# Performance work log

Hardware: AMD Instinct MI355X
Metric: run time of the kernel (lower is better)

## Reference

```python
import jax, jax.numpy as jnp
import numpy as np

N_NODES, N_EDGES, H = 25000, 400000, 64
EPS = 1e-15


def _norm(x):
    return jnp.sqrt(jnp.sum(x * x, axis=-1, keepdims=True))


def _projx(x, c):
    norm = _norm(x)
    max_norm = (1.0 - 1e-5) / jnp.sqrt(c)
    scale = jnp.minimum(max_norm / jnp.maximum(norm, EPS), 1.0)
    return x * scale


def _expmap0(x, c):
    norm = _norm(x)
    sc = jnp.sqrt(c)
    return jnp.tanh(sc * norm) * x / (norm * sc + EPS)


def _logmap0(x, c):
    norm = _norm(x)
    sc = jnp.sqrt(c)
    return (1.0 / sc) * jnp.arctanh(jnp.minimum(sc * norm, 1.0 - 1e-5)) * x / (norm + EPS)


def _mobius_add(x, y, c):
    x2 = jnp.sum(x * x, axis=-1, keepdims=True)
    y2 = jnp.sum(y * y, axis=-1, keepdims=True)
    xy = jnp.sum(x * y, axis=-1, keepdims=True)
    num = (1.0 + 2.0 * c * xy + c * y2) * x + (1.0 - c * x2) * y
    denom = 1.0 + 2.0 * c * xy + c * c * x2 * y2
    return num / (denom + EPS)


def _mobius_linear(x, W, b, c):
    t = _logmap0(x, c)
    out = t @ W.T + b
    return _expmap0(out, c)


def setup_inputs() -> dict:
    key = jax.random.key(0)
    ks = jax.random.split(key, 12)
    h_V = jax.random.normal(ks[0], (N_NODES, H), dtype=jnp.float32) * 0.3
    h_E = jax.random.normal(ks[1], (N_EDGES, 3 * H), dtype=jnp.float32) * 0.3
    src = jax.random.randint(ks[2], (N_EDGES,), 0, N_NODES, dtype=jnp.int32)
    dst = jax.random.randint(ks[3], (N_EDGES,), 0, N_NODES, dtype=jnp.int32)
    log_c = jnp.zeros((), dtype=jnp.float32)  # c = 1.0

    def lin(k, out_d, in_d):
        bound = 1.0 / np.sqrt(in_d)
        kw, kb = jax.random.split(k)
        W = jax.random.uniform(kw, (out_d, in_d), jnp.float32, -bound, bound)
        b = jax.random.uniform(kb, (out_d,), jnp.float32, -bound, bound)
        return W, b

    W1_w, W1_b = lin(ks[4], H, 5 * H)
    W2_w, W2_b = lin(ks[5], H, H)
    W3_w, W3_b = lin(ks[6], H, H)
    return {"h_V": h_V, "h_E": h_E, "src": src, "dst": dst, "log_c": log_c,
            "W1_w": W1_w, "W1_b": W1_b, "W2_w": W2_w, "W2_b": W2_b,
            "W3_w": W3_w, "W3_b": W3_b}


def reference(h_V, h_E, src, dst, log_c, W1_w, W1_b, W2_w, W2_b, W3_w, W3_b):
    c = jnp.exp(log_c)
    n_nodes = h_V.shape[0]
    h_E = _projx(h_E, c)
    h_V = _projx(h_V, c)
    # edge gather -> fused mobius-linear chain  [E, 5H] -> [E, H]
    h_EV = jnp.concatenate([h_E, h_V[src], h_V[dst]], axis=-1)
    h_EV = _mobius_linear(h_EV, W1_w, W1_b, c)
    h_EV = _mobius_linear(_projx(jax.nn.relu(h_EV), c), W2_w, W2_b, c)
    h_msg = _mobius_linear(_projx(jax.nn.relu(h_EV), c), W3_w, W3_b, c)
    # hyperbolic aggregate: logmap0 -> scatter-mean over src -> expmap0
    tangent = _logmap0(h_msg, c)
    sums = jax.ops.segment_sum(tangent, src, num_segments=n_nodes)
    counts = jax.ops.segment_sum(jnp.ones((tangent.shape[0],), tangent.dtype), src,
                                 num_segments=n_nodes)
    agg_t = sums / jnp.maximum(counts, 1.0)[:, None]
    agg = _expmap0(agg_t, c)
    h_V = _mobius_add(h_V, agg, c)  # dropout disabled (eval)
    return _projx(h_V, c)
```

## Files before the change

kernel.cpp:

```cpp
#include <hip/hip_runtime.h>
#include <hip/hip_bf16.h>
#include <math.h>

#define EPSF 1e-15f

typedef __attribute__((ext_vector_type(8))) short bf16x8;
typedef __attribute__((ext_vector_type(16))) float f32x16;

__device__ __forceinline__ unsigned short f2bf(float x) {
    unsigned u = __float_as_uint(x);
    u += 0x7fffu + ((u >> 16) & 1u);
    return (unsigned short)(u >> 16);
}
__device__ __forceinline__ float bf2f(unsigned short b) {
    return __uint_as_float(((unsigned)b) << 16);
}
__device__ __forceinline__ unsigned pkbf(float lo, float hi) {
    __hip_bfloat162 h = __float22bfloat162_rn(make_float2(lo, hi));
    return *reinterpret_cast<unsigned*>(&h);
}
__device__ __forceinline__ float fast_tanh_pos(float x) {
    if (x < 0.25f) { float x2 = x * x; return x * (1.0f - x2 * (0.33333334f - 0.13333334f * x2)); }
    float e = __expf(2.0f * x);
    return 1.0f - 2.0f / (e + 1.0f);
}
__device__ __forceinline__ float fast_atanh01(float y) {
    if (y < 0.125f) { float y2 = y * y; return y * (1.0f + y2 * (0.33333334f + 0.2f * y2)); }
    return 0.5f * __logf((1.0f + y) / (1.0f - y));
}

__device__ __forceinline__ float wred(float v) {
#pragma unroll
    for (int off = 32; off; off >>= 1) v += __shfl_xor(v, off);
    return v;
}

__global__ void prep_wfrag(const float* __restrict__ W1, const float* __restrict__ W2,
                           const float* __restrict__ W3, unsigned short* __restrict__ Wf) {
    int idx = blockIdx.x * blockDim.x + threadIdx.x;
    if (idx >= 56 * 64) return;
    int fid = idx >> 6, lane = idx & 63;
    int e31 = lane & 31, hi = lane >> 5;
    unsigned short* dstp = Wf + ((size_t)fid * 64 + lane) * 8;
    if (fid < 40) {
        int ks = fid >> 1, t = fid & 1;
        int n = 32 * t + e31;
        int k0 = 16 * ks + 8 * hi;
#pragma unroll
        for (int i = 0; i < 8; ++i) dstp[i] = f2bf(W1[n * 320 + k0 + i]);
    } else {
        const float* srcW = (fid < 48) ? W2 : W3;
        int b = (fid < 48) ? fid - 40 : fid - 48;
        int ks = b >> 1, t2 = b & 1;
        int n = 32 * t2 + e31;
        int cb = 32 * (ks >> 1) + 16 * (ks & 1) + 4 * hi;
#pragma unroll
        for (int i = 0; i < 8; ++i) dstp[i] = f2bf(srcW[n * 64 + cb + 8 * (i >> 2) + (i & 3)]);
    }
}

__global__ void __launch_bounds__(256)
node_prep(const float* __restrict__ hV, const float* __restrict__ logc,
          unsigned short* __restrict__ hVp, float* __restrict__ pj, int n_nodes) {
    int wid  = (blockIdx.x * blockDim.x + threadIdx.x) >> 6;
    int lane = threadIdx.x & 63;
    if (wid >= n_nodes) return;
    float c    = __expf(logc[0]);
    float scq  = sqrtf(c);
    float maxn = (1.0f - 1e-5f) / scq;
    float x = hV[(size_t)wid * 64 + lane];
    float p = wred(x * x);
    float sS = fminf(maxn / fmaxf(sqrtf(p), EPSF), 1.0f);
    hVp[(size_t)wid * 64 + lane] = f2bf(x * sS);
    if (lane == 0) pj[wid] = sS * sS * p;
}

__global__ void hist_kernel(const int* __restrict__ src, int* __restrict__ cnt,
                            int* __restrict__ slot, int n_edges) {
    int e = blockIdx.x * blockDim.x + threadIdx.x;
    if (e < n_edges) slot[e] = atomicAdd(&cnt[src[e]], 1);
}

__global__ void __launch_bounds__(1024)
scan_rowptr(const int* __restrict__ cnt, int* __restrict__ rowptr, int n) {
    __shared__ int wpart[16];
    int C   = (n + 1023) >> 10;
    int tid = threadIdx.x;
    int beg = tid * C;
    int end = beg + C; if (end > n) end = n;
    int s = 0;
    if (beg < n) for (int k = beg; k < end; ++k) s += cnt[k];
    int lane = tid & 63, wv = tid >> 6;
    int v = s;
#pragma unroll
    for (int off = 1; off < 64; off <<= 1) {
        int t = __shfl_up(v, off);
        if (lane >= off) v += t;
    }
    if (lane == 63) wpart[wv] = v;
    __syncthreads();
    if (tid < 64) {
        int t = (tid < 16) ? wpart[tid] : 0;
#pragma unroll
        for (int off = 1; off < 16; off <<= 1) {
            int u = __shfl_up(t, off);
            if (lane >= off) t += u;
        }
        if (tid < 16) wpart[tid] = t;
    }
    __syncthreads();
    int base = (wv ? wpart[wv - 1] : 0) + (v - s);
    if (beg < n) {
        int run = base;
        for (int k = beg; k < end; ++k) { rowptr[k] = run; run += cnt[k]; }
    }
    if (tid == 1023) rowptr[n] = wpart[15];
}

__global__ void __launch_bounds__(256, 4)
gemm1e(const float* __restrict__ hE, const unsigned short* __restrict__ Wf,
       unsigned short* __restrict__ yEb, float* __restrict__ pEarr,
       int n_edges, int n_tiles) {
    int lane = threadIdx.x & 63;
    int w    = threadIdx.x >> 6;
    int tile = blockIdx.x * 4 + w;
    if (tile >= n_tiles) return;
    int e31 = lane & 31, hi = lane >> 5;
    int ev = tile * 32 + e31; if (ev >= n_edges) ev = n_edges - 1;

    const bf16x8* Wfrag = reinterpret_cast<const bf16x8*>(Wf);
    const float* eb = hE + (size_t)ev * 192 + 8 * hi;

    f32x16 acc[2] = {};
    float pE = 0.f;
#pragma unroll 1
    for (int ks = 0; ks < 12; ++ks) {
        const float4* p4 = reinterpret_cast<const float4*>(eb + 16 * ks);
        float4 a0 = p4[0], a1 = p4[1];
        pE += a0.x*a0.x + a0.y*a0.y + a0.z*a0.z + a0.w*a0.w
            + a1.x*a1.x + a1.y*a1.y + a1.z*a1.z + a1.w*a1.w;
        union { bf16x8 b; unsigned u[4]; } cv;
        cv.u[0] = pkbf(a0.x, a0.y);
        cv.u[1] = pkbf(a0.z, a0.w);
        cv.u[2] = pkbf(a1.x, a1.y);
        cv.u[3] = pkbf(a1.z, a1.w);
        acc[0] = __builtin_amdgcn_mfma_f32_32x32x16_bf16(
            Wfrag[(size_t)(ks * 2 + 0) * 64 + lane], cv.b, acc[0], 0, 0, 0);
        acc[1] = __builtin_amdgcn_mfma_f32_32x32x16_bf16(
            Wfrag[(size_t)(ks * 2 + 1) * 64 + lane], cv.b, acc[1], 0, 0, 0);
    }
    pE += __shfl_xor(pE, 32);

    unsigned pk[16];
#pragma unroll
    for (int t = 0; t < 2; ++t)
#pragma unroll
        for (int wd = 0; wd < 8; ++wd)
            pk[t * 8 + wd] = pkbf(acc[t][2 * wd], acc[t][2 * wd + 1]);
    uint4* op = reinterpret_cast<uint4*>(yEb + ((size_t)tile * 64 + lane) * 32);
    op[0] = make_uint4(pk[0],  pk[1],  pk[2],  pk[3]);
    op[1] = make_uint4(pk[4],  pk[5],  pk[6],  pk[7]);
    op[2] = make_uint4(pk[8],  pk[9],  pk[10], pk[11]);
    op[3] = make_uint4(pk[12], pk[13], pk[14], pk[15]);
    if (hi == 0 && tile * 32 + e31 < n_edges) pEarr[tile * 32 + e31] = pE;
}

__device__ __forceinline__ void stage_mlp32(float (&v)[2][16],
                                            const unsigned short* WfL, int fbase,
                                            const float* __restrict__ bvec,
                                            float scq, float maxn, int lane, int hi) {
    float n2 = 0.f, rn2 = 0.f;
    float u[2][16];
#pragma unroll
    for (int t = 0; t < 2; ++t)
#pragma unroll
        for (int j = 0; j < 16; ++j) {
            float x = v[t][j];
            n2 = fmaf(x, x, n2);
            float y = fmaxf(x, 0.f);
            u[t][j] = y;
            rn2 = fmaf(y, y, rn2);
        }
    n2  += __shfl_xor(n2, 32);
    rn2 += __shfl_xor(rn2, 32);
    float n  = sqrtf(n2);
    float h  = fast_tanh_pos(scq * n) / (n * scq + EPSF);
    float rn = h * sqrtf(rn2);
    float ps = fminf(maxn / fmaxf(rn, EPSF), 1.0f);
    float pn = rn * ps;
    float gg = fast_atanh01(fminf(scq * pn, 1.0f - 1e-5f)) / (scq * (pn + EPSF));
    float f2 = h * ps * gg;

    f32x16 acc[2] = {};
#pragma unroll
    for (int ks = 0; ks < 4; ++ks) {
        int t = ks >> 1, jb = 8 * (ks & 1);
        union { bf16x8 b; unsigned w[4]; } B;
        B.w[0] = pkbf(u[t][jb + 0], u[t][jb + 1]);
        B.w[1] = pkbf(u[t][jb + 2], u[t][jb + 3]);
        B.w[2] = pkbf(u[t][jb + 4], u[t][jb + 5]);
        B.w[3] = pkbf(u[t][jb + 6], u[t][jb + 7]);
#pragma unroll
        for (int t2 = 0; t2 < 2; ++t2) {
            bf16x8 wf = *reinterpret_cast<const bf16x8*>(
                &WfL[((fbase + ks * 2 + t2) * 64 + lane) * 8]);
            acc[t2] = __builtin_amdgcn_mfma_f32_32x32x16_bf16(wf, B.b, acc[t2], 0, 0, 0);
        }
    }
#pragma unroll
    for (int t2 = 0; t2 < 2; ++t2)
#pragma unroll
        for (int q = 0; q < 4; ++q) {
            const float4 bv = *reinterpret_cast<const float4*>(&bvec[32 * t2 + 8 * q + 4 * hi]);
            v[t2][4 * q + 0] = fmaf(f2, acc[t2][4 * q + 0], bv.x);
            v[t2][4 * q + 1] = fmaf(f2, acc[t2][4 * q + 1], bv.y);
            v[t2][4 * q + 2] = fmaf(f2, acc[t2][4 * q + 2], bv.z);
            v[t2][4 * q + 3] = fmaf(f2, acc[t2][4 * q + 3], bv.w);
        }
}

__global__ void __launch_bounds__(256, 4)
edge_mfma(const unsigned short* __restrict__ yEb, const float* __restrict__ pEarr,
          const int* __restrict__ src, const int* __restrict__ dst,
          const float* __restrict__ logc,
          const unsigned short* __restrict__ Wf, const unsigned short* __restrict__ hVp,
          const float* __restrict__ pj,
          const float* __restrict__ b1, const float* __restrict__ b2,
          const float* __restrict__ b3, const int* __restrict__ slot_,
          const int* __restrict__ rowptr,
          unsigned short* __restrict__ tg, int n_edges, int n_tiles) {
    __shared__ __align__(16) unsigned short WfL[16384];
    {
        const uint4* wsrc = reinterpret_cast<const uint4*>(Wf) + 1536;
        uint4* wdst = reinterpret_cast<uint4*>(WfL);
#pragma unroll
        for (int i = 0; i < 8; ++i)
            wdst[i * 256 + threadIdx.x] = wsrc[i * 256 + threadIdx.x];
    }
    __syncthreads();

    int lane = threadIdx.x & 63;
    int w    = threadIdx.x >> 6;
    int tile = blockIdx.x * 4 + w;
    if (tile >= n_tiles) return;

    float c    = __expf(logc[0]);
    float scq  = sqrtf(c);
    float maxn = (1.0f - 1e-5f) / scq;

    int e31 = lane & 31, hi = lane >> 5;
    int ev = tile * 32 + e31; if (ev >= n_edges) ev = n_edges - 1;
    int s16 = src[ev], d16 = dst[ev];
    int sl = slot_[ev] + rowptr[s16];
    float pjS = pj[s16], pjD = pj[d16];
    float pE  = pEarr[ev];

    const uint4* yp = reinterpret_cast<const uint4*>(yEb + ((size_t)tile * 64 + lane) * 32);
    uint4 y0 = yp[0], y1 = yp[1], y2 = yp[2], y3 = yp[3];
    unsigned yw[16] = { y0.x, y0.y, y0.z, y0.w, y1.x, y1.y, y1.z, y1.w,
                        y2.x, y2.y, y2.z, y2.w, y3.x, y3.y, y3.z, y3.w };

    const bf16x8* vsp = reinterpret_cast<const bf16x8*>(hVp + (size_t)s16 * 64);
    const bf16x8* vdp = reinterpret_cast<const bf16x8*>(hVp + (size_t)d16 * 64);
    bf16x8 aS[4], aD[4];
#pragma unroll
    for (int q = 0; q < 4; ++q) { aS[q] = vsp[2 * q + hi]; aD[q] = vdp[2 * q + hi]; }

    f32x16 accV[2] = {};
#pragma unroll
    for (int q = 0; q < 4; ++q) {
#pragma unroll
        for (int t = 0; t < 2; ++t) {
            bf16x8 wf = *reinterpret_cast<const bf16x8*>(&WfL[((q * 2 + t) * 64 + lane) * 8]);
            accV[t] = __builtin_amdgcn_mfma_f32_32x32x16_bf16(wf, aS[q], accV[t], 0, 0, 0);
        }
    }
#pragma unroll
    for (int q = 0; q < 4; ++q) {
#pragma unroll
        for (int t = 0; t < 2; ++t) {
            bf16x8 wf = *reinterpret_cast<const bf16x8*>(&WfL[((8 + q * 2 + t) * 64 + lane) * 8]);
            accV[t] = __builtin_amdgcn_mfma_f32_32x32x16_bf16(wf, aD[q], accV[t], 0, 0, 0);
        }
    }

    float sE = fminf(maxn / fmaxf(sqrtf(pE), EPSF), 1.0f);
    float nt = sqrtf(sE * sE * pE + pjS + pjD);
    float gq = fast_atanh01(fminf(scq * nt, 1.0f - 1e-5f)) / (scq * (nt + EPSF));

    float v[2][16];
#pragma unroll
    for (int t = 0; t < 2; ++t)
#pragma unroll
        for (int q = 0; q < 4; ++q) {
            const float4 bv = *reinterpret_cast<const float4*>(&b1[32 * t + 8 * q + 4 * hi]);
#pragma unroll
            for (int j = 0; j < 4; ++j) {
                int f = t * 16 + q * 4 + j;
                float ye = bf2f((unsigned short)(yw[f >> 1] >> (16 * (f & 1))));
                float bb = (j == 0) ? bv.x : (j == 1) ? bv.y : (j == 2) ? bv.z : bv.w;
                v[t][q * 4 + j] = fmaf(gq, fmaf(sE, ye, accV[t][q * 4 + j]), bb);
            }
        }

    stage_mlp32(v, WfL, 16, b2, scq, maxn, lane, hi);
    stage_mlp32(v, WfL, 24, b3, scq, maxn, lane, hi);

    float n2 = 0.f;
#pragma unroll
    for (int t = 0; t < 2; ++t)
#pragma unroll
        for (int j = 0; j < 16; ++j) n2 = fmaf(v[t][j], v[t][j], n2);
    n2 += __shfl_xor(n2, 32);
    float n  = sqrtf(n2);
    float h  = fast_tanh_pos(scq * n) / (n * scq + EPSF);
    float hn = h * n;
    float g4 = fast_atanh01(fminf(scq * hn, 1.0f - 1e-5f)) / (scq * (hn + EPSF));
    float fT = g4 * h;

    if (tile * 32 + e31 < n_edges) {
        unsigned short* orow = tg + (size_t)sl * 64;
#pragma unroll
        for (int t = 0; t < 2; ++t)
#pragma unroll
            for (int q = 0; q < 4; ++q) {
                uint2 o;
                o.x = pkbf(fT * v[t][4*q+0], fT * v[t][4*q+1]);
                o.y = pkbf(fT * v[t][4*q+2], fT * v[t][4*q+3]);
                *reinterpret_cast<uint2*>(&orow[32 * t + 8 * q + 4 * hi]) = o;
            }
    }
}

__global__ void __launch_bounds__(256)
node_gather(const float* __restrict__ hV, const float* __restrict__ logc,
            const unsigned short* __restrict__ tg, const int* __restrict__ rowptr,
            float* __restrict__ out, int n_nodes) {
    int wid  = (blockIdx.x * blockDim.x + threadIdx.x) >> 6;
    int lane = threadIdx.x & 63;
    if (wid >= n_nodes) return;

    float c    = __expf(logc[0]);
    float scq  = sqrtf(c);
    float maxn = (1.0f - 1e-5f) / scq;

    int beg = rowptr[wid], end = rowptr[wid + 1];
    int g = lane >> 4, i15 = lane & 15;
    float s0 = 0.f, s1 = 0.f, s2 = 0.f, s3 = 0.f;
    for (int i = beg + g; i < end; i += 4) {
        uint2 p = *reinterpret_cast<const uint2*>(&tg[(size_t)i * 64 + i15 * 4]);
        s0 += bf2f((unsigned short)(p.x & 0xffff));
        s1 += bf2f((unsigned short)(p.x >> 16));
        s2 += bf2f((unsigned short)(p.y & 0xffff));
        s3 += bf2f((unsigned short)(p.y >> 16));
    }
    s0 += __shfl_xor(s0, 16); s0 += __shfl_xor(s0, 32);
    s1 += __shfl_xor(s1, 16); s1 += __shfl_xor(s1, 32);
    s2 += __shfl_xor(s2, 16); s2 += __shfl_xor(s2, 32);
    s3 += __shfl_xor(s3, 16); s3 += __shfl_xor(s3, 32);
    int srcl = lane >> 2;
    float a0 = __shfl(s0, srcl), a1 = __shfl(s1, srcl);
    float a2 = __shfl(s2, srcl), a3 = __shfl(s3, srcl);
    float ssum = (lane & 2) ? ((lane & 1) ? a3 : a2) : ((lane & 1) ? a1 : a0);

    float inv = 1.f / fmaxf((float)(end - beg), 1.f);
    float at  = ssum * inv;

    float an2 = wred(at * at);
    float an  = sqrtf(an2);
    float ae  = fast_tanh_pos(scq * an) / (an * scq + EPSF);

    float xv  = hV[(size_t)wid * 64 + lane];
    float hs2 = wred(xv * xv);
    float sX  = fminf(maxn / fmaxf(sqrtf(hs2), EPSF), 1.0f);

    float x = sX * xv, y = ae * at;
    float x2 = wred(x * x);
    float y2 = wred(y * y);
    float xy = wred(x * y);

    float ca = 1.f + 2.f * c * xy + c * y2;
    float cb = 1.f - c * x2;
    float id = 1.f / (1.f + 2.f * c * xy + c * c * x2 * y2 + EPSF);

    float r   = (ca * x + cb * y) * id;
    float rn2 = wred(r * r);
    float rs  = fminf(maxn / fmaxf(sqrtf(rn2), EPSF), 1.0f);

    out[(size_t)wid * 64 + lane] = rs * r;
}

extern "C" void kernel_launch(void* const* d_in, const int* in_sizes, int n_in,
                              void* d_out, int out_size, void* d_ws, size_t ws_size,
                              hipStream_t stream) {
    const float* hV   = (const float*)d_in[0];
    const float* hE   = (const float*)d_in[1];
    const int*   src  = (const int*)d_in[2];
    const int*   dst  = (const int*)d_in[3];
    const float* logc = (const float*)d_in[4];
    const float* W1   = (const float*)d_in[5];
    const float* b1   = (const float*)d_in[6];
    const float* W2   = (const float*)d_in[7];
    const float* b2   = (const float*)d_in[8];
    const float* W3   = (const float*)d_in[9];
    const float* b3   = (const float*)d_in[10];

    int n_nodes = in_sizes[0] / 64;
    int n_edges = in_sizes[2];
    int n_tiles = (n_edges + 31) / 32;
    float* out = (float*)d_out;

    char* wsb = (char*)d_ws;
    unsigned short* Wf = (unsigned short*)wsb;
    size_t off = 56 * 512 * sizeof(unsigned short);
    int* cnt    = (int*)(wsb + off);   off += (size_t)n_nodes * 4;
    int* rowptr = (int*)(wsb + off);   off += (size_t)(n_nodes + 1) * 4;
    int* slot   = (int*)(wsb + off);   off += (size_t)n_edges * 4;
    float* pj   = (float*)(wsb + off); off += (size_t)n_nodes * 4;
    float* pEarr= (float*)(wsb + off); off += (size_t)n_edges * 4;
    off = (off + 15) & ~(size_t)15;
    unsigned short* hVp = (unsigned short*)(wsb + off);
    off += (size_t)n_nodes * 64 * 2;
    off = (off + 15) & ~(size_t)15;
    unsigned short* yEb = (unsigned short*)(wsb + off);
    off += (size_t)n_tiles * 64 * 32 * 2;
    off = (off + 15) & ~(size_t)15;
    unsigned short* tg = (unsigned short*)(wsb + off);

    hipMemsetAsync(cnt, 0, (size_t)n_nodes * sizeof(int), stream);

    prep_wfrag<<<(56 * 64 + 255) / 256, 256, 0, stream>>>(W1, W2, W3, Wf);
    node_prep<<<(n_nodes + 3) / 4, 256, 0, stream>>>(hV, logc, hVp, pj, n_nodes);
    hist_kernel<<<(n_edges + 255) / 256, 256, 0, stream>>>(src, cnt, slot, n_edges);
    scan_rowptr<<<1, 1024, 0, stream>>>(cnt, rowptr, n_nodes);

    gemm1e<<<(n_tiles + 3) / 4, 256, 0, stream>>>(hE, Wf, yEb, pEarr, n_edges, n_tiles);

    edge_mfma<<<(n_tiles + 3) / 4, 256, 0, stream>>>(
        yEb, pEarr, src, dst, logc, Wf, hVp, pj, b1, b2, b3, slot, rowptr,
        tg, n_edges, n_tiles);

    node_gather<<<(n_nodes + 3) / 4, 256, 0, stream>>>(
        hV, logc, tg, rowptr, out, n_nodes);
}
```

Baseline: 251.4 us.

## Fuse edge-feature GEMM into the edge MLP kernel, dropping intermediate buffers

Merges the separate h_E projection kernel into the main edge kernel, so the bf16 intermediate yE and the per-edge squared norm are kept in registers instead of being written to and reread from global memory. This removes one launch and a round trip of about 26MB of intermediate traffic. The fused kernel now carries both the E-part and V-part accumulators at once, which raises register pressure and may lower occupancy. The E-part accumulator is also no longer rounded to bf16 before use.

```diff
diff --git a/kernel.cpp b/kernel.cpp
--- a/kernel.cpp
+++ b/kernel.cpp
@@ -117,21 +117,119 @@
     if (tid == 1023) rowptr[n] = wpart[15];
 }
 
+__device__ __forceinline__ void stage_mlp32(float (&v)[2][16],
+                                            const unsigned short* WfL, int fbase,
+                                            const float* __restrict__ bvec,
+                                            float scq, float maxn, int lane, int hi) {
+    float n2 = 0.f, rn2 = 0.f;
+    float u[2][16];
+#pragma unroll
+    for (int t = 0; t < 2; ++t)
+#pragma unroll
+        for (int j = 0; j < 16; ++j) {
+            float x = v[t][j];
+            n2 = fmaf(x, x, n2);
+            float y = fmaxf(x, 0.f);
+            u[t][j] = y;
+            rn2 = fmaf(y, y, rn2);
+        }
+    n2  += __shfl_xor(n2, 32);
+    rn2 += __shfl_xor(rn2, 32);
+    float n  = sqrtf(n2);
+    float h  = fast_tanh_pos(scq * n) / (n * scq + EPSF);
+    float rn = h * sqrtf(rn2);
+    float ps = fminf(maxn / fmaxf(rn, EPSF), 1.0f);
+    float pn = rn * ps;
+    float gg = fast_atanh01(fminf(scq * pn, 1.0f - 1e-5f)) / (scq * (pn + EPSF));
+    float f2 = h * ps * gg;
+
+    f32x16 acc[2] = {};
+#pragma unroll
+    for (int ks = 0; ks < 4; ++ks) {
+        int t = ks >> 1, jb = 8 * (ks & 1);
+        union { bf16x8 b; unsigned w[4]; } B;
+        B.w[0] = pkbf(u[t][jb + 0], u[t][jb + 1]);
+        B.w[1] = pkbf(u[t][jb + 2], u[t][jb + 3]);
+        B.w[2] = pkbf(u[t][jb + 4], u[t][jb + 5]);
+        B.w[3] = pkbf(u[t][jb + 6], u[t][jb + 7]);
+#pragma unroll
+        for (int t2 = 0; t2 < 2; ++t2) {
+            bf16x8 wf = *reinterpret_cast<const bf16x8*>(
+                &WfL[((fbase + ks * 2 + t2) * 64 + lane) * 8]);
+            acc[t2] = __builtin_amdgcn_mfma_f32_32x32x16_bf16(wf, B.b, acc[t2], 0, 0, 0);
+        }
+    }
+#pragma unroll
+    for (int t2 = 0; t2 < 2; ++t2)
+#pragma unroll
+        for (int q = 0; q < 4; ++q) {
+            const float4 bv = *reinterpret_cast<const float4*>(&bvec[32 * t2 + 8 * q + 4 * hi]);
+            v[t2][4 * q + 0] = fmaf(f2, acc[t2][4 * q + 0], bv.x);
+            v[t2][4 * q + 1] = fmaf(f2, acc[t2][4 * q + 1], bv.y);
+            v[t2][4 * q + 2] = fmaf(f2, acc[t2][4 * q + 2], bv.z);
+            v[t2][4 * q + 3] = fmaf(f2, acc[t2][4 * q + 3], bv.w);
+        }
+}
+
 __global__ void __launch_bounds__(256, 4)
-gemm1e(const float* __restrict__ hE, const unsigned short* __restrict__ Wf,
-       unsigned short* __restrict__ yEb, float* __restrict__ pEarr,
-       int n_edges, int n_tiles) {
+edge_fused(const float* __restrict__ hE, const int* __restrict__ src,
+           const int* __restrict__ dst, const float* __restrict__ logc,
+           const unsigned short* __restrict__ Wf, const unsigned short* __restrict__ hVp,
+           const float* __restrict__ pj,
+           const float* __restrict__ b1, const float* __restrict__ b2,
+           const float* __restrict__ b3, const int* __restrict__ slot_,
+           const int* __restrict__ rowptr,
+           unsigned short* __restrict__ tg, int n_edges, int n_tiles) {
+    __shared__ __align__(16) unsigned short WfL[16384];
+    {
+        const uint4* wsrc = reinterpret_cast<const uint4*>(Wf) + 1536;
+        uint4* wdst = reinterpret_cast<uint4*>(WfL);
+#pragma unroll
+        for (int i = 0; i < 8; ++i)
+            wdst[i * 256 + threadIdx.x] = wsrc[i * 256 + threadIdx.x];
+    }
+    __syncthreads();
+
     int lane = threadIdx.x & 63;
     int w    = threadIdx.x >> 6;
     int tile = blockIdx.x * 4 + w;
     if (tile >= n_tiles) return;
+
+    float c    = __expf(logc[0]);
+    float scq  = sqrtf(c);
+    float maxn = (1.0f - 1e-5f) / scq;
+
     int e31 = lane & 31, hi = lane >> 5;
     int ev = tile * 32 + e31; if (ev >= n_edges) ev = n_edges - 1;
+    int s16 = src[ev], d16 = dst[ev];
+    int sl = slot_[ev] + rowptr[s16];
+    float pjS = pj[s16], pjD = pj[d16];
+
+    const bf16x8* vsp = reinterpret_cast<const bf16x8*>(hVp + (size_t)s16 * 64);
+    const bf16x8* vdp = reinterpret_cast<const bf16x8*>(hVp + (size_t)d16 * 64);
+    f32x16 accV[2] = {};
+#pragma unroll
+    for (int q = 0; q < 4; ++q) {
+        bf16x8 aS = vsp[2 * q + hi];
+#pragma unroll
+        for (int t = 0; t < 2; ++t) {
+            bf16x8 wf = *reinterpret_cast<const bf16x8*>(&WfL[((q * 2 + t) * 64 + lane) * 8]);
+            accV[t] = __builtin_amdgcn_mfma_f32_32x32x16_bf16(wf, aS, accV[t], 0, 0, 0);
+        }
+    }
+#pragma unroll
+    for (int q = 0; q < 4; ++q) {
+        bf16x8 aD = vdp[2 * q + hi];
+#pragma unroll
+        for (int t = 0; t < 2; ++t) {
+            bf16x8 wf = *reinterpret_cast<const bf16x8*>(&WfL[((8 + q * 2 + t) * 64 + lane) * 8]);
+            accV[t] = __builtin_amdgcn_mfma_f32_32x32x16_bf16(wf, aD, accV[t], 0, 0, 0);
+        }
+    }
 
     const bf16x8* Wfrag = reinterpret_cast<const bf16x8*>(Wf);
     const float* eb = hE + (size_t)ev * 192 + 8 * hi;
-
-    f32x16 acc[2] = {};
+    f32x16 accE[2] = {};
     float pE = 0.f;
 #pragma unroll 1
     for (int ks = 0; ks < 12; ++ks) {
@@ -144,145 +242,12 @@
         cv.u[1] = pkbf(a0.z, a0.w);
         cv.u[2] = pkbf(a1.x, a1.y);
         cv.u[3] = pkbf(a1.z, a1.w);
-        acc[0] = __builtin_amdgcn_mfma_f32_32x32x16_bf16(
-            Wfrag[(size_t)(ks * 2 + 0) * 64 + lane], cv.b, acc[0], 0, 0, 0);
-        acc[1] = __builtin_amdgcn_mfma_f32_32x32x16_bf16(
-            Wfrag[(size_t)(ks * 2 + 1) * 64 + lane], cv.b, acc[1], 0, 0, 0);
+        accE[0] = __builtin_amdgcn_mfma_f32_32x32x16_bf16(
+            Wfrag[(size_t)(ks * 2 + 0) * 64 + lane], cv.b, accE[0], 0, 0, 0);
+        accE[1] = __builtin_amdgcn_mfma_f32_32x32x16_bf16(
+            Wfrag[(size_t)(ks * 2 + 1) * 64 + lane], cv.b, accE[1], 0, 0, 0);
     }
     pE += __shfl_xor(pE, 32);
-
-    unsigned pk[16];
-#pragma unroll
-    for (int t = 0; t < 2; ++t)
-#pragma unroll
-        for (int wd = 0; wd < 8; ++wd)
-            pk[t * 8 + wd] = pkbf(acc[t][2 * wd], acc[t][2 * wd + 1]);
-    uint4* op = reinterpret_cast<uint4*>(yEb + ((size_t)tile * 64 + lane) * 32);
-    op[0] = make_uint4(pk[0],  pk[1],  pk[2],  pk[3]);
-    op[1] = make_uint4(pk[4],  pk[5],  pk[6],  pk[7]);
-    op[2] = make_uint4(pk[8],  pk[9],  pk[10], pk[11]);
-    op[3] = make_uint4(pk[12], pk[13], pk[14], pk[15]);
-    if (hi == 0 && tile * 32 + e31 < n_edges) pEarr[tile * 32 + e31] = pE;
-}
-
-__device__ __forceinline__ void stage_mlp32(float (&v)[2][16],
-                                            const unsigned short* WfL, int fbase,
-                                            const float* __restrict__ bvec,
-                                            float scq, float maxn, int lane, int hi) {
-    float n2 = 0.f, rn2 = 0.f;
-    float u[2][16];
-#pragma unroll
-    for (int t = 0; t < 2; ++t)
-#pragma unroll
-        for (int j = 0; j < 16; ++j) {
-            float x = v[t][j];
-            n2 = fmaf(x, x, n2);
-            float y = fmaxf(x, 0.f);
-            u[t][j] = y;
-            rn2 = fmaf(y, y, rn2);
-        }
-    n2  += __shfl_xor(n2, 32);
-    rn2 += __shfl_xor(rn2, 32);
-    float n  = sqrtf(n2);
-    float h  = fast_tanh_pos(scq * n) / (n * scq + EPSF);
-    float rn = h * sqrtf(rn2);
-    float ps = fminf(maxn / fmaxf(rn, EPSF), 1.0f);
-    float pn = rn * ps;
-    float gg = fast_atanh01(fminf(scq * pn, 1.0f - 1e-5f)) / (scq * (pn + EPSF));
-    float f2 = h * ps * gg;
-
-    f32x16 acc[2] = {};
-#pragma unroll
-    for (int ks = 0; ks < 4; ++ks) {
-        int t = ks >> 1, jb = 8 * (ks & 1);
-        union { bf16x8 b; unsigned w[4]; } B;
-        B.w[0] = pkbf(u[t][jb + 0], u[t][jb + 1]);
-        B.w[1] = pkbf(u[t][jb + 2], u[t][jb + 3]);
-        B.w[2] = pkbf(u[t][jb + 4], u[t][jb + 5]);
-        B.w[3] = pkbf(u[t][jb + 6], u[t][jb + 7]);
-#pragma unroll
-        for (int t2 = 0; t2 < 2; ++t2) {
-            bf16x8 wf = *reinterpret_cast<const bf16x8*>(
-                &WfL[((fbase + ks * 2 + t2) * 64 + lane) * 8]);
-            acc[t2] = __builtin_amdgcn_mfma_f32_32x32x16_bf16(wf, B.b, acc[t2], 0, 0, 0);
-        }
-    }
-#pragma unroll
-    for (int t2 = 0; t2 < 2; ++t2)
-#pragma unroll
-        for (int q = 0; q < 4; ++q) {
-            const float4 bv = *reinterpret_cast<const float4*>(&bvec[32 * t2 + 8 * q + 4 * hi]);
-            v[t2][4 * q + 0] = fmaf(f2, acc[t2][4 * q + 0], bv.x);
-            v[t2][4 * q + 1] = fmaf(f2, acc[t2][4 * q + 1], bv.y);
-            v[t2][4 * q + 2] = fmaf(f2, acc[t2][4 * q + 2], bv.z);
-            v[t2][4 * q + 3] = fmaf(f2, acc[t2][4 * q + 3], bv.w);
-        }
-}
-
-__global__ void __launch_bounds__(256, 4)
-edge_mfma(const unsigned short* __restrict__ yEb, const float* __restrict__ pEarr,
-          const int* __restrict__ src, const int* __restrict__ dst,
-          const float* __restrict__ logc,
-          const unsigned short* __restrict__ Wf, const unsigned short* __restrict__ hVp,
-          const float* __restrict__ pj,
-          const float* __restrict__ b1, const float* __restrict__ b2,
-          const float* __restrict__ b3, const int* __restrict__ slot_,
-          const int* __restrict__ rowptr,
-          unsigned short* __restrict__ tg, int n_edges, int n_tiles) {
-    __shared__ __align__(16) unsigned short WfL[16384];
-    {
-        const uint4* wsrc = reinterpret_cast<const uint4*>(Wf) + 1536;
-        uint4* wdst = reinterpret_cast<uint4*>(WfL);
-#pragma unroll
-        for (int i = 0; i < 8; ++i)
-            wdst[i * 256 + threadIdx.x] = wsrc[i * 256 + threadIdx.x];
-    }
-    __syncthreads();
-
-    int lane = threadIdx.x & 63;
-    int w    = threadIdx.x >> 6;
-    int tile = blockIdx.x * 4 + w;
-    if (tile >= n_tiles) return;
-
-    float c    = __expf(logc[0]);
-    float scq  = sqrtf(c);
-    float maxn = (1.0f - 1e-5f) / scq;
-
-    int e31 = lane & 31, hi = lane >> 5;
-    int ev = tile * 32 + e31; if (ev >= n_edges) ev = n_edges - 1;
-    int s16 = src[ev], d16 = dst[ev];
-    int sl = slot_[ev] + rowptr[s16];
-    float pjS = pj[s16], pjD = pj[d16];
-    float pE  = pEarr[ev];
-
-    const uint4* yp = reinterpret_cast<const uint4*>(yEb + ((size_t)tile * 64 + lane) * 32);
-    uint4 y0 = yp[0], y1 = yp[1], y2 = yp[2], y3 = yp[3];
-    unsigned yw[16] = { y0.x, y0.y, y0.z, y0.w, y1.x, y1.y, y1.z, y1.w,
-                        y2.x, y2.y, y2.z, y2.w, y3.x, y3.y, y3.z, y3.w };
-
-    const bf16x8* vsp = reinterpret_cast<const bf16x8*>(hVp + (size_t)s16 * 64);
-    const bf16x8* vdp = reinterpret_cast<const bf16x8*>(hVp + (size_t)d16 * 64);
-    bf16x8 aS[4], aD[4];
-#pragma unroll
-    for (int q = 0; q < 4; ++q) { aS[q] = vsp[2 * q + hi]; aD[q] = vdp[2 * q + hi]; }
-
-    f32x16 accV[2] = {};
-#pragma unroll
-    for (int q = 0; q < 4; ++q) {
-#pragma unroll
-        for (int t = 0; t < 2; ++t) {
-            bf16x8 wf = *reinterpret_cast<const bf16x8*>(&WfL[((q * 2 + t) * 64 + lane) * 8]);
-            accV[t] = __builtin_amdgcn_mfma_f32_32x32x16_bf16(wf, aS[q], accV[t], 0, 0, 0);
-        }
-    }
-#pragma unroll
-    for (int q = 0; q < 4; ++q) {
-#pragma unroll
-        for (int t = 0; t < 2; ++t) {
-            bf16x8 wf = *reinterpret_cast<const bf16x8*>(&WfL[((8 + q * 2 + t) * 64 + lane) * 8]);
-            accV[t] = __builtin_amdgcn_mfma_f32_32x32x16_bf16(wf, aD[q], accV[t], 0, 0, 0);
-        }
-    }
 
     float sE = fminf(maxn / fmaxf(sqrtf(pE), EPSF), 1.0f);
     float nt = sqrtf(sE * sE * pE + pjS + pjD);
@@ -294,13 +259,10 @@
 #pragma unroll
         for (int q = 0; q < 4; ++q) {
             const float4 bv = *reinterpret_cast<const float4*>(&b1[32 * t + 8 * q + 4 * hi]);
-#pragma unroll
-            for (int j = 0; j < 4; ++j) {
-                int f = t * 16 + q * 4 + j;
-                float ye = bf2f((unsigned short)(yw[f >> 1] >> (16 * (f & 1))));
-                float bb = (j == 0) ? bv.x : (j == 1) ? bv.y : (j == 2) ? bv.z : bv.w;
-                v[t][q * 4 + j] = fmaf(gq, fmaf(sE, ye, accV[t][q * 4 + j]), bb);
-            }
+            v[t][4*q+0] = fmaf(gq, fmaf(sE, accE[t][4*q+0], accV[t][4*q+0]), bv.x);
+            v[t][4*q+1] = fmaf(gq, fmaf(sE, accE[t][4*q+1], accV[t][4*q+1]), bv.y);
+            v[t][4*q+2] = fmaf(gq, fmaf(sE, accE[t][4*q+2], accV[t][4*q+2]), bv.z);
+            v[t][4*q+3] = fmaf(gq, fmaf(sE, accE[t][4*q+3], accV[t][4*q+3]), bv.w);
         }
 
     stage_mlp32(v, WfL, 16, b2, scq, maxn, lane, hi);
@@ -417,14 +379,10 @@
     int* rowptr = (int*)(wsb + off);   off += (size_t)(n_nodes + 1) * 4;
     int* slot   = (int*)(wsb + off);   off += (size_t)n_edges * 4;
     float* pj   = (float*)(wsb + off); off += (size_t)n_nodes * 4;
-    float* pEarr= (float*)(wsb + off); off += (size_t)n_edges * 4;
     off = (off + 15) & ~(size_t)15;
     unsigned short* hVp = (unsigned short*)(wsb + off);
     off += (size_t)n_nodes * 64 * 2;
     off = (off + 15) & ~(size_t)15;
-    unsigned short* yEb = (unsigned short*)(wsb + off);
-    off += (size_t)n_tiles * 64 * 32 * 2;
-    off = (off + 15) & ~(size_t)15;
     unsigned short* tg = (unsigned short*)(wsb + off);
 
     hipMemsetAsync(cnt, 0, (size_t)n_nodes * sizeof(int), stream);
@@ -434,10 +392,8 @@
     hist_kernel<<<(n_edges + 255) / 256, 256, 0, stream>>>(src, cnt, slot, n_edges);
     scan_rowptr<<<1, 1024, 0, stream>>>(cnt, rowptr, n_nodes);
 
-    gemm1e<<<(n_tiles + 3) / 4, 256, 0, stream>>>(hE, Wf, yEb, pEarr, n_edges, n_tiles);
-
-    edge_mfma<<<(n_tiles + 3) / 4, 256, 0, stream>>>(
-        yEb, pEarr, src, dst, logc, Wf, hVp, pj, b1, b2, b3, slot, rowptr,
+    edge_fused<<<(n_tiles + 3) / 4, 256, 0, stream>>>(
+        hE, src, dst, logc, Wf, hVp, pj, b1, b2, b3, slot, rowptr,
         tg, n_edges, n_tiles);
 
     node_gather<<<(n_nodes + 3) / 4, 256, 0, stream>>>(
```

New measurement: 240.1 us. 1.05x faster.
